# Kernel optimization log

Hardware: AMD Instinct MI355X
Metric: run time of the kernel (lower is better)

Reference implementation:

```python
import jax, jax.numpy as jnp
import numpy as np

B, N, C, H = 8, 4096, 1024, 16
D = C // H            # head_dim = 64
SCALE = D ** -0.5


def setup_inputs() -> dict:
    key = jax.random.key(0)
    k1, k2, k3 = jax.random.split(key, 3)
    x = jax.random.normal(k1, (B, N, C), dtype=jnp.float32)
    w_qkv = jax.random.normal(k2, (C, 3 * C), dtype=jnp.float32) * 0.02
    w_proj = jax.random.normal(k3, (C, C), dtype=jnp.float32) * 0.02
    b_proj = jnp.zeros((C,), dtype=jnp.float32)
    return {"x": x, "w_qkv": w_qkv, "w_proj": w_proj, "b_proj": b_proj}


def reference(x, w_qkv, w_proj, b_proj):
    # Faithful translation of the TF module, INCLUDING its missing head-permute:
    # after unstack, q/k/v are (B, N, H, D); tf.matmul batches over (B, N),
    # so attention is an (H x H) softmax over heads, per token.
    Bv, Nv, Cv = x.shape
    qkv = (x @ w_qkv).reshape(Bv, Nv, 3, H, D)          # qkv has no bias (qkv_bias=False)
    q, k, v = qkv[:, :, 0], qkv[:, :, 1], qkv[:, :, 2]   # each (B, N, H, D)
    q = q * SCALE
    attn = jnp.einsum("bnhd,bngd->bnhg", q, k)           # (B, N, H, H)
    attn = jax.nn.softmax(attn, axis=-1)
    o = jnp.einsum("bnhg,bngd->bnhd", attn, v)           # (B, N, H, D)
    o = jnp.transpose(o, (0, 2, 1, 3)).reshape(Bv, Nv, Cv)  # literal transpose+reshape
    return o @ w_proj + b_proj
```

## Files before the change

kernel.cpp:

```cpp
#include <hip/hip_runtime.h>
#include <hip/hip_bf16.h>
#include <stdint.h>

typedef __attribute__((ext_vector_type(8))) short short8;
typedef __attribute__((ext_vector_type(4))) float f32x4;
typedef unsigned short ushort_t;

#define VMCNT4 asm volatile("s_waitcnt vmcnt(4)" ::: "memory")
#define VMCNT0 asm volatile("s_waitcnt vmcnt(0)" ::: "memory")
#define LGKM0  asm volatile("s_waitcnt lgkmcnt(0)" ::: "memory")
#define BARRIER asm volatile("s_barrier" ::: "memory")

__device__ inline ushort_t f2bf(float f) {
    union { float f; unsigned u; } v; v.f = f;
    unsigned u = v.u;
    unsigned r = u + 0x7fffu + ((u >> 16) & 1u);
    return (ushort_t)(r >> 16);
}

__device__ inline void gload_lds16(const void* g, void* l) {
    __builtin_amdgcn_global_load_lds((const __attribute__((address_space(1))) void*)g,
                                     (__attribute__((address_space(3))) void*)l,
                                     16, 0, 0);
}

__device__ inline short8 read_frag(const ushort_t* region, int r, int c) {
    int byte = (r << 7) + (c << 1);
    byte ^= (r & 7) << 4;
    return *(const short8*)((const char*)region + byte);
}

#define MFMA16(MB, NB, BF)                                                        \
    _Pragma("unroll")                                                             \
    for (int mi = 0; mi < 4; ++mi)                                                \
        _Pragma("unroll")                                                         \
        for (int ni = 0; ni < 2; ++ni)                                            \
            _Pragma("unroll")                                                     \
            for (int ks = 0; ks < 2; ++ks)                                        \
                acc[(MB) + mi][(NB) + ni] = __builtin_amdgcn_mfma_f32_16x16x32_bf16( \
                    aF[mi * 2 + ks], BF[ni * 2 + ks], acc[(MB) + mi][(NB) + ni], 0, 0, 0);

template <int F32OUT>
__global__ __launch_bounds__(512, 2) void gemm256(const ushort_t* __restrict__ A,
                                                  const ushort_t* __restrict__ Bt,
                                                  void* __restrict__ Cc,
                                                  const float* __restrict__ bias,
                                                  int N, int K, int NBN) {
    __shared__ __align__(16) ushort_t lds[65536];
    const int tid = threadIdx.x;
    const int wave = tid >> 6;
    const int lane = tid & 63;
    const int wm = wave >> 2;
    const int wn = wave & 3;
    const int el = (lane & 56) | ((lane ^ (lane >> 3)) & 7);

    const int nwg = gridDim.x;
    const int bid = (int)blockIdx.x;
    const int x = (bid & 7) * (nwg >> 3) + (bid >> 3);
    const int per = NBN << 3;
    const int st = x / per;
    const int rem = x - st * per;
    const int bn = rem >> 3;
    const int bm = (st << 3) + (rem & 7);

    const ushort_t* Ag = A + (size_t)bm * 256 * K;
    const ushort_t* Bg = Bt + (size_t)bn * 256 * K;
    const int NT = K >> 6;

    auto STAGE = [&](const ushort_t* g, int rowHalf, int k0, int regionByteOff) {
#pragma unroll
        for (int j = 0; j < 2; ++j) {
            int e = j * 4096 + wave * 512 + el * 8;
            gload_lds16(g + (size_t)(rowHalf + (e >> 6)) * K + k0 + (e & 63),
                        (char*)lds + regionByteOff + j * 8192 + wave * 1024);
        }
    };

    STAGE(Ag, 0,   0, 0);
    STAGE(Ag, 128, 0, 16384);
    STAGE(Bg, 0,   0, 65536);
    STAGE(Bg, 128, 0, 65536 + 16384);
    STAGE(Bg, 0,   64, 65536 + 32768);
    STAGE(Bg, 128, 64, 65536 + 49152);
    VMCNT4;
    BARRIER;

    f32x4 acc[8][4] = {};
    short8 aF[8], bF0[4], bF1[4];
    const int ra = lane & 15;
    const int ca = (lane >> 4) << 3;
    const int rb = (wn & 1) << 6;

    for (int it = 0; it < NT; ++it) {
        const int s = it & 1;
        const ushort_t* Ar = lds + ((s << 1) + wm) * 8192;
        const ushort_t* Br = lds + 32768 + ((s << 1) + (wn >> 1)) * 8192;
        const bool doA = (it + 1) < NT;
        const bool doB = (it + 2) < NT;
        const int kA = (it + 1) << 6;
        const int kB = (it + 2) << 6;
        const int soA = ((s ^ 1) << 1) * 16384;
        const int soB = 65536 + (s << 1) * 16384;

#pragma unroll
        for (int mi = 0; mi < 4; ++mi)
#pragma unroll
            for (int ks = 0; ks < 2; ++ks)
                aF[mi * 2 + ks] = read_frag(Ar, mi * 16 + ra, ks * 32 + ca);
#pragma unroll
        for (int ni = 0; ni < 2; ++ni)
#pragma unroll
            for (int ks = 0; ks < 2; ++ks)
                bF0[ni * 2 + ks] = read_frag(Br, rb + ni * 16 + ra, ks * 32 + ca);
        if (doA) STAGE(Ag, 0, kA, soA);
        BARRIER; LGKM0;
        __builtin_amdgcn_s_setprio(1);
        MFMA16(0, 0, bF0)
        __builtin_amdgcn_s_setprio(0);

#pragma unroll
        for (int ni = 0; ni < 2; ++ni)
#pragma unroll
            for (int ks = 0; ks < 2; ++ks)
                bF1[ni * 2 + ks] = read_frag(Br, rb + 32 + ni * 16 + ra, ks * 32 + ca);
        if (doA) STAGE(Ag, 128, kA, soA + 16384);
        BARRIER; LGKM0;
        __builtin_amdgcn_s_setprio(1);
        MFMA16(0, 2, bF1)
        __builtin_amdgcn_s_setprio(0);

#pragma unroll
        for (int mi = 0; mi < 4; ++mi)
#pragma unroll
            for (int ks = 0; ks < 2; ++ks)
                aF[mi * 2 + ks] = read_frag(Ar, 64 + mi * 16 + ra, ks * 32 + ca);
        BARRIER; LGKM0;
        if (doB) STAGE(Bg, 0, kB, soB);
        __builtin_amdgcn_s_setprio(1);
        MFMA16(4, 0, bF0)
        __builtin_amdgcn_s_setprio(0);

        if (doB) STAGE(Bg, 128, kB, soB + 16384);
        __builtin_amdgcn_s_setprio(1);
        MFMA16(4, 2, bF1)
        __builtin_amdgcn_s_setprio(0);
        if (doB) { VMCNT4; } else { VMCNT0; }
        BARRIER;
    }

    const int row0 = bm * 256 + wm * 128 + (lane >> 4) * 4;
    const int col0 = bn * 256 + wn * 64 + (lane & 15);
#pragma unroll
    for (int mi = 0; mi < 8; ++mi) {
#pragma unroll
        for (int ni = 0; ni < 4; ++ni) {
            const int col = col0 + ni * 16;
            f32x4 v = acc[mi][ni];
            if constexpr (F32OUT) {
                float bz = bias[col];
                float* C = (float*)Cc;
#pragma unroll
                for (int q = 0; q < 4; ++q)
                    C[(size_t)(row0 + mi * 16 + q) * N + col] = v[q] + bz;
            } else {
                ushort_t* C = (ushort_t*)Cc;
#pragma unroll
                for (int q = 0; q < 4; ++q)
                    C[(size_t)(row0 + mi * 16 + q) * N + col] = f2bf(v[q]);
            }
        }
    }
}

__global__ __launch_bounds__(256) void cast_x_kernel(const float* __restrict__ in,
                                                     ushort_t* __restrict__ out,
                                                     int n8) {
    int i = blockIdx.x * blockDim.x + threadIdx.x;
    int stride = gridDim.x * blockDim.x;
    for (; i < n8; i += stride) {
        const float4* p = (const float4*)(in + (size_t)i * 8);
        float4 a = p[0];
        float4 b = p[1];
        uint4 w;
        w.x = (unsigned)f2bf(a.x) | ((unsigned)f2bf(a.y) << 16);
        w.y = (unsigned)f2bf(a.z) | ((unsigned)f2bf(a.w) << 16);
        w.z = (unsigned)f2bf(b.x) | ((unsigned)f2bf(b.y) << 16);
        w.w = (unsigned)f2bf(b.z) | ((unsigned)f2bf(b.w) << 16);
        *(uint4*)(out + (size_t)i * 8) = w;
    }
}

__global__ __launch_bounds__(256) void transpose_cast_kernel(const float* __restrict__ in,
                                                             ushort_t* __restrict__ out,
                                                             int R, int Cn) {
    __shared__ float tile[64][65];
    int t = threadIdx.x;
    int c0 = blockIdx.x * 64;
    int r0 = blockIdx.y * 64;
    int lr = t >> 4;
    int lc = (t & 15) * 4;
#pragma unroll
    for (int i = 0; i < 4; i++) {
        const float* src = in + (size_t)(r0 + i * 16 + lr) * Cn + c0 + lc;
        float4 v = *(const float4*)src;
        tile[i * 16 + lr][lc + 0] = v.x;
        tile[i * 16 + lr][lc + 1] = v.y;
        tile[i * 16 + lr][lc + 2] = v.z;
        tile[i * 16 + lr][lc + 3] = v.w;
    }
    __syncthreads();
    int oc = t >> 4;
    int ok = (t & 15) * 4;
#pragma unroll
    for (int i = 0; i < 4; i++) {
        int c = c0 + i * 16 + oc;
        ushort4 w;
        w.x = f2bf(tile[ok + 0][i * 16 + oc]);
        w.y = f2bf(tile[ok + 1][i * 16 + oc]);
        w.z = f2bf(tile[ok + 2][i * 16 + oc]);
        w.w = f2bf(tile[ok + 3][i * 16 + oc]);
        *(ushort4*)(out + (size_t)c * R + r0 + ok) = w;
    }
}

__global__ __launch_bounds__(256) void attn_kernel(const ushort_t* __restrict__ qkv,
                                                   ushort_t* __restrict__ operm) {
    __shared__ __align__(16) float plds[4][16 * 20];
    const int wave = threadIdx.x >> 6;
    const int lane = threadIdx.x & 63;
    float* P = plds[wave];
    const int fr = lane & 15;
    const int fo = (lane >> 4) * 8;
    int tok = (blockIdx.x * 4 + wave) * 4;
    for (int it = 0; it < 4; it++, tok++) {
        const ushort_t* row = qkv + (size_t)tok * 3072;
        short8 aq0 = *(const short8*)(row + fr * 64 + fo);
        short8 aq1 = *(const short8*)(row + fr * 64 + 32 + fo);
        short8 bk0 = *(const short8*)(row + 1024 + fr * 64 + fo);
        short8 bk1 = *(const short8*)(row + 1024 + fr * 64 + 32 + fo);
        f32x4 s = {0.f, 0.f, 0.f, 0.f};
        s = __builtin_amdgcn_mfma_f32_16x16x32_bf16(aq0, bk0, s, 0, 0, 0);
        s = __builtin_amdgcn_mfma_f32_16x16x32_bf16(aq1, bk1, s, 0, 0, 0);
        float ls[4], m[4], p[4], sm[4];
#pragma unroll
        for (int q = 0; q < 4; q++) { ls[q] = s[q] * 0.125f; m[q] = ls[q]; }
#pragma unroll
        for (int d = 1; d < 16; d <<= 1)
#pragma unroll
            for (int q = 0; q < 4; q++) m[q] = fmaxf(m[q], __shfl_xor(m[q], d));
#pragma unroll
        for (int q = 0; q < 4; q++) { p[q] = __expf(ls[q] - m[q]); sm[q] = p[q]; }
#pragma unroll
        for (int d = 1; d < 16; d <<= 1)
#pragma unroll
            for (int q = 0; q < 4; q++) sm[q] += __shfl_xor(sm[q], d);
#pragma unroll
        for (int q = 0; q < 4; q++) P[((lane >> 4) * 4 + q) * 20 + fr] = p[q];
        __syncthreads();
        short8 pa = {};
        if (lane < 32) {
            const float* src = P + fr * 20 + fo;
            float4 r0 = *(const float4*)src;
            float4 r1 = *(const float4*)(src + 4);
            pa[0] = (short)f2bf(r0.x); pa[1] = (short)f2bf(r0.y);
            pa[2] = (short)f2bf(r0.z); pa[3] = (short)f2bf(r0.w);
            pa[4] = (short)f2bf(r1.x); pa[5] = (short)f2bf(r1.y);
            pa[6] = (short)f2bf(r1.z); pa[7] = (short)f2bf(r1.w);
        }
        __syncthreads();
        f32x4 o[4] = {};
        const ushort_t* vrow = row + 2048;
#pragma unroll
        for (int db = 0; db < 4; db++) {
            short8 bv = {};
            if (lane < 32) {
#pragma unroll
                for (int j = 0; j < 8; j++)
                    bv[j] = (short)vrow[(fo + j) * 64 + db * 16 + fr];
            }
            o[db] = __builtin_amdgcn_mfma_f32_16x16x32_bf16(pa, bv, o[db], 0, 0, 0);
        }
        float inv[4];
#pragma unroll
        for (int q = 0; q < 4; q++) inv[q] = 1.0f / sm[q];
        int b = tok >> 12;
        int n = tok & 4095;
        ushort_t* obase = operm + ((size_t)b << 22);
        int rlo = n >> 4;
        int cbase = (n & 15) * 64;
#pragma unroll
        for (int db = 0; db < 4; db++) {
#pragma unroll
            for (int q = 0; q < 4; q++) {
                int h = (lane >> 4) * 4 + q;
                int d = db * 16 + fr;
                obase[(size_t)(h * 256 + rlo) * 1024 + cbase + d] = f2bf(o[db][q] * inv[q]);
            }
        }
    }
}

extern "C" void kernel_launch(void* const* d_in, const int* in_sizes, int n_in,
                              void* d_out, int out_size, void* d_ws, size_t ws_size,
                              hipStream_t stream) {
    const float* x = (const float*)d_in[0];
    const float* w_qkv = (const float*)d_in[1];
    const float* w_proj = (const float*)d_in[2];
    const float* b_proj = (const float*)d_in[3];
    float* out = (float*)d_out;

    char* ws = (char*)d_ws;
    ushort_t* x_bf  = (ushort_t*)(ws);
    ushort_t* wq_t  = (ushort_t*)(ws + 67108864);
    ushort_t* wp_t  = (ushort_t*)(ws + 73400320);
    ushort_t* qkv   = (ushort_t*)(ws + 75497472);
    ushort_t* operm = (ushort_t*)(ws + 276824064);

    cast_x_kernel<<<2048, 256, 0, stream>>>(x, x_bf, 33554432 / 8);
    transpose_cast_kernel<<<dim3(48, 16), 256, 0, stream>>>(w_qkv, wq_t, 1024, 3072);
    transpose_cast_kernel<<<dim3(16, 16), 256, 0, stream>>>(w_proj, wp_t, 1024, 1024);
    gemm256<0><<<1536, 512, 0, stream>>>(x_bf, wq_t, qkv, nullptr, 3072, 1024, 12);
    attn_kernel<<<2048, 256, 0, stream>>>(qkv, operm);
    gemm256<1><<<512, 512, 0, stream>>>(operm, wp_t, out, b_proj, 1024, 1024, 4);
}
```

Measured before the change: 397.6 us.

## Make GEMM kernels persistent and prefetch the next tile across tile boundaries

Both GEMMs become persistent kernels launched with 256 workgroups, each looping over logical tiles with stride 256. The double-buffered K pipeline carries over between tiles: the last iterations of one tile stage the first K-slices of the next tile, so the prologue load latency is overlapped and launch tail effects shrink. The cost is extra address selection per iteration, a serialized epilogue between tiles, and reliance on K being a power-of-two multiple of 64 for the wrap mask. With 256 CUs and launch bounds of 2 blocks per CU, only half of the possible occupancy is used.

```diff
diff --git a/kernel.cpp b/kernel.cpp
--- a/kernel.cpp
+++ b/kernel.cpp
@@ -45,7 +45,7 @@
                                                   const ushort_t* __restrict__ Bt,
                                                   void* __restrict__ Cc,
                                                   const float* __restrict__ bias,
-                                                  int N, int K, int NBN) {
+                                                  int N, int K, int NBN, int LT) {
     __shared__ __align__(16) ushort_t lds[65536];
     const int tid = threadIdx.x;
     const int wave = tid >> 6;
@@ -53,19 +53,17 @@
     const int wm = wave >> 2;
     const int wn = wave & 3;
     const int el = (lane & 56) | ((lane ^ (lane >> 3)) & 7);
-
-    const int nwg = gridDim.x;
-    const int bid = (int)blockIdx.x;
-    const int x = (bid & 7) * (nwg >> 3) + (bid >> 3);
-    const int per = NBN << 3;
-    const int st = x / per;
-    const int rem = x - st * per;
-    const int bn = rem >> 3;
-    const int bm = (st << 3) + (rem & 7);
-
-    const ushort_t* Ag = A + (size_t)bm * 256 * K;
-    const ushort_t* Bg = Bt + (size_t)bn * 256 * K;
     const int NT = K >> 6;
+    const int NTM = NT - 1;
+
+    auto tile_of = [&](int lt, int& obm, int& obn) {
+        int x = (lt & 7) * (LT >> 3) + (lt >> 3);
+        int per = NBN << 3;
+        int st = x / per;
+        int rem = x - st * per;
+        obn = rem >> 3;
+        obm = (st << 3) + (rem & 7);
+    };
 
     auto STAGE = [&](const ushort_t* g, int rowHalf, int k0, int regionByteOff) {
 #pragma unroll
@@ -75,6 +73,11 @@
                         (char*)lds + regionByteOff + j * 8192 + wave * 1024);
         }
     };
+
+    int bm, bn;
+    tile_of((int)blockIdx.x, bm, bn);
+    const ushort_t* Ag = A + (size_t)bm * 256 * K;
+    const ushort_t* Bg = Bt + (size_t)bn * 256 * K;
 
     STAGE(Ag, 0,   0, 0);
     STAGE(Ag, 128, 0, 16384);
@@ -87,88 +90,106 @@
 
     f32x4 acc[8][4] = {};
     short8 aF[8], bF0[4], bF1[4];
+    const f32x4 zf = {0.f, 0.f, 0.f, 0.f};
     const int ra = lane & 15;
     const int ca = (lane >> 4) << 3;
     const int rb = (wn & 1) << 6;
 
-    for (int it = 0; it < NT; ++it) {
-        const int s = it & 1;
-        const ushort_t* Ar = lds + ((s << 1) + wm) * 8192;
-        const ushort_t* Br = lds + 32768 + ((s << 1) + (wn >> 1)) * 8192;
-        const bool doA = (it + 1) < NT;
-        const bool doB = (it + 2) < NT;
-        const int kA = (it + 1) << 6;
-        const int kB = (it + 2) << 6;
-        const int soA = ((s ^ 1) << 1) * 16384;
-        const int soB = 65536 + (s << 1) * 16384;
-
-#pragma unroll
-        for (int mi = 0; mi < 4; ++mi)
-#pragma unroll
-            for (int ks = 0; ks < 2; ++ks)
-                aF[mi * 2 + ks] = read_frag(Ar, mi * 16 + ra, ks * 32 + ca);
-#pragma unroll
-        for (int ni = 0; ni < 2; ++ni)
-#pragma unroll
-            for (int ks = 0; ks < 2; ++ks)
-                bF0[ni * 2 + ks] = read_frag(Br, rb + ni * 16 + ra, ks * 32 + ca);
-        if (doA) STAGE(Ag, 0, kA, soA);
-        BARRIER; LGKM0;
-        __builtin_amdgcn_s_setprio(1);
-        MFMA16(0, 0, bF0)
-        __builtin_amdgcn_s_setprio(0);
-
-#pragma unroll
-        for (int ni = 0; ni < 2; ++ni)
-#pragma unroll
-            for (int ks = 0; ks < 2; ++ks)
-                bF1[ni * 2 + ks] = read_frag(Br, rb + 32 + ni * 16 + ra, ks * 32 + ca);
-        if (doA) STAGE(Ag, 128, kA, soA + 16384);
-        BARRIER; LGKM0;
-        __builtin_amdgcn_s_setprio(1);
-        MFMA16(0, 2, bF1)
-        __builtin_amdgcn_s_setprio(0);
-
-#pragma unroll
-        for (int mi = 0; mi < 4; ++mi)
-#pragma unroll
-            for (int ks = 0; ks < 2; ++ks)
-                aF[mi * 2 + ks] = read_frag(Ar, 64 + mi * 16 + ra, ks * 32 + ca);
-        BARRIER; LGKM0;
-        if (doB) STAGE(Bg, 0, kB, soB);
-        __builtin_amdgcn_s_setprio(1);
-        MFMA16(4, 0, bF0)
-        __builtin_amdgcn_s_setprio(0);
-
-        if (doB) STAGE(Bg, 128, kB, soB + 16384);
-        __builtin_amdgcn_s_setprio(1);
-        MFMA16(4, 2, bF1)
-        __builtin_amdgcn_s_setprio(0);
-        if (doB) { VMCNT4; } else { VMCNT0; }
-        BARRIER;
-    }
-
-    const int row0 = bm * 256 + wm * 128 + (lane >> 4) * 4;
-    const int col0 = bn * 256 + wn * 64 + (lane & 15);
-#pragma unroll
-    for (int mi = 0; mi < 8; ++mi) {
-#pragma unroll
-        for (int ni = 0; ni < 4; ++ni) {
-            const int col = col0 + ni * 16;
-            f32x4 v = acc[mi][ni];
-            if constexpr (F32OUT) {
-                float bz = bias[col];
-                float* C = (float*)Cc;
-#pragma unroll
-                for (int q = 0; q < 4; ++q)
-                    C[(size_t)(row0 + mi * 16 + q) * N + col] = v[q] + bz;
-            } else {
-                ushort_t* C = (ushort_t*)Cc;
-#pragma unroll
-                for (int q = 0; q < 4; ++q)
-                    C[(size_t)(row0 + mi * 16 + q) * N + col] = f2bf(v[q]);
+    for (int lt = (int)blockIdx.x; lt < LT; lt += 256) {
+        const bool hasN = (lt + 256) < LT;
+        int bmN = bm, bnN = bn;
+        const ushort_t* AgN = Ag;
+        const ushort_t* BgN = Bg;
+        if (hasN) {
+            tile_of(lt + 256, bmN, bnN);
+            AgN = A + (size_t)bmN * 256 * K;
+            BgN = Bt + (size_t)bnN * 256 * K;
+        }
+
+        for (int it = 0; it < NT; ++it) {
+            const int s = it & 1;
+            const ushort_t* Ar = lds + ((s << 1) + wm) * 8192;
+            const ushort_t* Br = lds + 32768 + ((s << 1) + (wn >> 1)) * 8192;
+            const int itA = it + 1, itB = it + 2;
+            const bool doA = (itA < NT) || hasN;
+            const bool doB = (itB < NT) || hasN;
+            const ushort_t* As = (itA < NT) ? Ag : AgN;
+            const ushort_t* Bs = (itB < NT) ? Bg : BgN;
+            const int kA = (itA & NTM) << 6;
+            const int kB = (itB & NTM) << 6;
+            const int soA = ((s ^ 1) << 1) * 16384;
+            const int soB = 65536 + (s << 1) * 16384;
+
+#pragma unroll
+            for (int mi = 0; mi < 4; ++mi)
+#pragma unroll
+                for (int ks = 0; ks < 2; ++ks)
+                    aF[mi * 2 + ks] = read_frag(Ar, mi * 16 + ra, ks * 32 + ca);
+#pragma unroll
+            for (int ni = 0; ni < 2; ++ni)
+#pragma unroll
+                for (int ks = 0; ks < 2; ++ks)
+                    bF0[ni * 2 + ks] = read_frag(Br, rb + ni * 16 + ra, ks * 32 + ca);
+            if (doA) STAGE(As, 0, kA, soA);
+            BARRIER; LGKM0;
+            __builtin_amdgcn_s_setprio(1);
+            MFMA16(0, 0, bF0)
+            __builtin_amdgcn_s_setprio(0);
+
+#pragma unroll
+            for (int ni = 0; ni < 2; ++ni)
+#pragma unroll
+                for (int ks = 0; ks < 2; ++ks)
+                    bF1[ni * 2 + ks] = read_frag(Br, rb + 32 + ni * 16 + ra, ks * 32 + ca);
+            if (doA) STAGE(As, 128, kA, soA + 16384);
+            BARRIER; LGKM0;
+            __builtin_amdgcn_s_setprio(1);
+            MFMA16(0, 2, bF1)
+            __builtin_amdgcn_s_setprio(0);
+
+#pragma unroll
+            for (int mi = 0; mi < 4; ++mi)
+#pragma unroll
+                for (int ks = 0; ks < 2; ++ks)
+                    aF[mi * 2 + ks] = read_frag(Ar, 64 + mi * 16 + ra, ks * 32 + ca);
+            BARRIER; LGKM0;
+            if (doB) STAGE(Bs, 0, kB, soB);
+            __builtin_amdgcn_s_setprio(1);
+            MFMA16(4, 0, bF0)
+            __builtin_amdgcn_s_setprio(0);
+
+            if (doB) STAGE(Bs, 128, kB, soB + 16384);
+            __builtin_amdgcn_s_setprio(1);
+            MFMA16(4, 2, bF1)
+            __builtin_amdgcn_s_setprio(0);
+            if (doB) { VMCNT4; } else { VMCNT0; }
+            BARRIER;
+        }
+
+        const int row0 = bm * 256 + wm * 128 + (lane >> 4) * 4;
+        const int col0 = bn * 256 + wn * 64 + (lane & 15);
+#pragma unroll
+        for (int mi = 0; mi < 8; ++mi) {
+#pragma unroll
+            for (int ni = 0; ni < 4; ++ni) {
+                const int col = col0 + ni * 16;
+                f32x4 v = acc[mi][ni];
+                if constexpr (F32OUT) {
+                    float bz = bias[col];
+                    float* C = (float*)Cc;
+#pragma unroll
+                    for (int q = 0; q < 4; ++q)
+                        C[(size_t)(row0 + mi * 16 + q) * N + col] = v[q] + bz;
+                } else {
+                    ushort_t* C = (ushort_t*)Cc;
+#pragma unroll
+                    for (int q = 0; q < 4; ++q)
+                        C[(size_t)(row0 + mi * 16 + q) * N + col] = f2bf(v[q]);
+                }
+                acc[mi][ni] = zf;
             }
         }
+        Ag = AgN; Bg = BgN; bm = bmN; bn = bnN;
     }
 }
 
@@ -319,7 +340,7 @@
     cast_x_kernel<<<2048, 256, 0, stream>>>(x, x_bf, 33554432 / 8);
     transpose_cast_kernel<<<dim3(48, 16), 256, 0, stream>>>(w_qkv, wq_t, 1024, 3072);
     transpose_cast_kernel<<<dim3(16, 16), 256, 0, stream>>>(w_proj, wp_t, 1024, 1024);
-    gemm256<0><<<1536, 512, 0, stream>>>(x_bf, wq_t, qkv, nullptr, 3072, 1024, 12);
+    gemm256<0><<<256, 512, 0, stream>>>(x_bf, wq_t, qkv, nullptr, 3072, 1024, 12, 1536);
     attn_kernel<<<2048, 256, 0, stream>>>(qkv, operm);
-    gemm256<1><<<512, 512, 0, stream>>>(operm, wp_t, out, b_proj, 1024, 1024, 4);
-}
+    gemm256<1><<<256, 512, 0, stream>>>(operm, wp_t, out, b_proj, 1024, 1024, 4, 512);
+}
```

Measured after the change: 389.0 us. 1.02x faster.
